# Kernel tuning notes

Measured on AMD Instinct MI355X. Metric: run time of the kernel, lower is better.

The kernel has to match this reference:

```python
import jax, jax.numpy as jnp
import numpy as np

B, A, N, G, F = 16, 256, 64, 64, 128  # batch, atoms, neighbors, gaussians, filters
CUTOFF = 5.0


def ssp(x):
    # shifted softplus: ln(0.5*e^x + 0.5)
    return jax.nn.softplus(x) - jnp.log(2.0).astype(x.dtype)


def setup_inputs() -> dict:
    key = jax.random.key(0)
    ks = jax.random.split(key, 10)
    x = jax.random.normal(ks[0], (B, A, F), jnp.float32)
    r_ij = jax.random.uniform(ks[1], (B, A, N), jnp.float32) * 6.0  # some beyond cutoff
    f_ij = jax.random.uniform(ks[2], (B, A, N, G), jnp.float32)  # gaussian-expanded dists
    neighbors = jax.random.randint(ks[3], (B, A, N), 0, A)
    pairwise_mask = (jax.random.uniform(ks[4], (B, A, N)) < 0.9).astype(jnp.float32)
    s = lambda fan: 1.0 / np.sqrt(fan)
    fw1 = jax.random.normal(ks[5], (G, F), jnp.float32) * s(G)
    fb1 = jnp.zeros((F,), jnp.float32)
    fw2 = jax.random.normal(ks[6], (F, F), jnp.float32) * s(F)
    fb2 = jnp.zeros((F,), jnp.float32)
    w_in2f = jax.random.normal(ks[7], (F, F), jnp.float32) * s(F)
    w_f2out = jax.random.normal(ks[8], (F, F), jnp.float32) * s(F)
    b_f2out = jnp.zeros((F,), jnp.float32)
    return {"x": x, "r_ij": r_ij, "f_ij": f_ij, "neighbors": neighbors,
            "pairwise_mask": pairwise_mask, "fw1": fw1, "fb1": fb1, "fw2": fw2,
            "fb2": fb2, "w_in2f": w_in2f, "w_f2out": w_f2out, "b_f2out": b_f2out}


def reference(x, r_ij, f_ij, neighbors, pairwise_mask,
              fw1, fb1, fw2, fb2, w_in2f, w_f2out, b_f2out):
    # filter network: Dense(G->F, ssp) -> Dense(F->F)
    W = ssp(jnp.einsum('bang,gf->banf', f_ij, fw1) + fb1)
    W = jnp.einsum('banf,fh->banh', W, fw2) + fb2  # [B,A,N,F]
    # cosine cutoff
    C = 0.5 * (jnp.cos(r_ij * (jnp.pi / CUTOFF)) + 1.0)
    C = C * (r_ij < CUTOFF).astype(r_ij.dtype)
    W = W * C[..., None]
    # in2f (no bias), then gather neighbor features along atom axis
    y = jnp.einsum('bad,df->baf', x, w_in2f)  # [B,A,F]
    bidx = jnp.arange(y.shape[0])[:, None, None]
    y_nbh = y[bidx, neighbors]  # [B,A,N,F]
    # filter-weight multiply + masked sum aggregate over neighbor axis
    y = jnp.sum(y_nbh * W * pairwise_mask[..., None], axis=2)  # [B,A,F]
    # f2out with shifted-softplus activation
    return ssp(jnp.einsum('baf,fo->bao', y, w_f2out) + b_f2out)
```

## Files before the change

### kernel.cpp

```cpp
#include <hip/hip_runtime.h>
#include <hip/hip_bf16.h>
#include <math.h>

#define B_ 16
#define A_ 256
#define N_ 64
#define G_ 64
#define F_ 128

typedef __attribute__((ext_vector_type(8))) short short8;
typedef __attribute__((ext_vector_type(4))) float floatx4;

__device__ __forceinline__ float ssp(float x) {
    const float t = __expf(-fabsf(x));
    return fmaxf(x, 0.0f) + __logf(1.0f + t) - 0.69314718055994531f;
}
__device__ __forceinline__ unsigned f2bf(float f) {
    union { float f; unsigned u; } v; v.f = f;
    v.u += 0x7fffu + ((v.u >> 16) & 1u);
    return v.u >> 16;
}
__device__ __forceinline__ float bf2f_lo(unsigned d) {
    union { unsigned i; float f; } v; v.i = d << 16; return v.f;
}
__device__ __forceinline__ float bf2f_hi(unsigned d) {
    union { unsigned i; float f; } v; v.i = d & 0xffff0000u; return v.f;
}

__global__ __launch_bounds__(256) void k0_repack(
    const float* __restrict__ fw1, const float* __restrict__ fw2,
    const float* __restrict__ win, const float* __restrict__ wout,
    unsigned short* __restrict__ fw1B, unsigned short* __restrict__ fw2B,
    unsigned short* __restrict__ winB, unsigned short* __restrict__ woutB)
{
    int idx = blockIdx.x * 1024 + threadIdx.x * 4;
    #pragma unroll
    for (int u = 0; u < 4; ++u, ++idx) {
        if (idx < 8192) {
            const int j  = idx & 7;
            const int l  = (idx >> 3) & 63;
            const int ks = (idx >> 9) & 1;
            const int tf = idx >> 10;
            const int g  = ks * 32 + (l >> 4) * 8 + j;
            const int f  = tf * 16 + (l & 15);
            fw1B[idx] = (unsigned short)f2bf(fw1[g * F_ + f]);
        } else {
            const int i2  = (idx - 8192) & 16383;
            const int sel = (idx - 8192) >> 14;
            const int j  = i2 & 7;
            const int l  = (i2 >> 3) & 63;
            const int ks = (i2 >> 9) & 3;
            const int tf = i2 >> 11;
            const int k  = ks * 32 + (l >> 4) * 8 + j;
            const int f  = tf * 16 + (l & 15);
            const float v = (sel == 0) ? fw2[k * F_ + f]
                          : (sel == 1) ? win[k * F_ + f]
                                       : wout[k * F_ + f];
            unsigned short* dst = (sel == 0) ? fw2B : (sel == 1) ? winB : woutB;
            dst[i2] = (unsigned short)f2bf(v);
        }
    }
}

__global__ __launch_bounds__(256) void in2f_gemm(
    const float* __restrict__ x, const unsigned short* __restrict__ winB,
    unsigned short* __restrict__ ypre)
{
    const int tid = threadIdx.x;
    const int w = tid >> 6, l = tid & 63, quad = l >> 4, c0 = l & 15;
    const int row = blockIdx.x * 64 + w * 16 + c0;

    short8 a[4];
    {
        const float* base = x + (size_t)row * F_ + quad * 8;
        #pragma unroll
        for (int ks = 0; ks < 4; ++ks) {
            const float4 v0 = *(const float4*)(base + ks * 32);
            const float4 v1 = *(const float4*)(base + ks * 32 + 4);
            short8 t;
            t[0] = (short)f2bf(v0.x); t[1] = (short)f2bf(v0.y);
            t[2] = (short)f2bf(v0.z); t[3] = (short)f2bf(v0.w);
            t[4] = (short)f2bf(v1.x); t[5] = (short)f2bf(v1.y);
            t[6] = (short)f2bf(v1.z); t[7] = (short)f2bf(v1.w);
            a[ks] = t;
        }
    }

    const short8* W8 = (const short8*)winB;
    floatx4 acc[8];
    #pragma unroll
    for (int tf = 0; tf < 8; ++tf) acc[tf] = (floatx4){0.f,0.f,0.f,0.f};
    #pragma unroll
    for (int ks = 0; ks < 4; ++ks)
        #pragma unroll
        for (int tf = 0; tf < 8; ++tf)
            acc[tf] = __builtin_amdgcn_mfma_f32_16x16x32_bf16(
                a[ks], W8[(tf * 4 + ks) * 64 + l], acc[tf], 0, 0, 0);

    #pragma unroll
    for (int r = 0; r < 4; ++r) {
        const int ro = blockIdx.x * 64 + w * 16 + quad * 4 + r;
        short8 s;
        #pragma unroll
        for (int tf = 0; tf < 8; ++tf) s[tf] = (short)f2bf(acc[tf][r]);
        *(short8*)&ypre[(size_t)ro * F_ + c0 * 8] = s;
    }
}

__global__ __launch_bounds__(512) void cfconv_kernel(
    const float* __restrict__ r_ij, const float* __restrict__ f_ij,
    const int*   __restrict__ nbrs, const float* __restrict__ mask,
    const float* __restrict__ fb1,  const float* __restrict__ fb2,
    const unsigned short* __restrict__ ypre,
    const unsigned short* __restrict__ fw1B,
    const unsigned short* __restrict__ fw2B,
    unsigned short* __restrict__ y_agg)
{
    __shared__ unsigned short s_w[24576];
    __shared__ short s_h1[N_ * F_];
    __shared__ float s_scale[N_];
    __shared__ int   s_nb[N_];
    __shared__ float s_red[4][F_];

    const int blk  = blockIdx.x;
    const int tid  = threadIdx.x;
    const int b    = blk >> 8;
    const int w    = tid >> 6;
    const int l    = tid & 63;
    const int quad = l >> 4;
    const int c0   = l & 15;
    const int rw   = w & 3;
    const int h    = w >> 2;

    {
        const uint4* w1 = (const uint4*)fw1B;
        const uint4* w2 = (const uint4*)fw2B;
        uint4* dst = (uint4*)s_w;
        #pragma unroll
        for (int i = 0; i < 6; ++i) {
            const int idx = tid + i * 512;
            dst[idx] = (idx < 1024) ? w1[idx] : w2[idx - 1024];
        }
    }
    if (h == 0 && l < 16) {
        const int n = rw * 16 + l;
        const float r = r_ij[(size_t)blk * N_ + n];
        const float c = (r < 5.0f)
            ? 0.5f * (__cosf(r * 0.62831853071795865f) + 1.0f)
            : 0.0f;
        s_scale[n] = c * mask[(size_t)blk * N_ + n];
        s_nb[n]    = nbrs[(size_t)blk * N_ + n];
    }

    short8 a1[2];
    {
        const float* base = f_ij + (size_t)blk * (N_ * G_)
                          + (size_t)(rw * 16 + c0) * G_ + quad * 8;
        #pragma unroll
        for (int ks = 0; ks < 2; ++ks) {
            const float4 v0 = *(const float4*)(base + ks * 32);
            const float4 v1 = *(const float4*)(base + ks * 32 + 4);
            short8 a;
            a[0] = (short)f2bf(v0.x); a[1] = (short)f2bf(v0.y);
            a[2] = (short)f2bf(v0.z); a[3] = (short)f2bf(v0.w);
            a[4] = (short)f2bf(v1.x); a[5] = (short)f2bf(v1.y);
            a[6] = (short)f2bf(v1.z); a[7] = (short)f2bf(v1.w);
            a1[ks] = a;
        }
    }
    __syncthreads();

    const short8* sw1 = (const short8*)s_w;
    const short8* sw2 = (const short8*)(s_w + 8192);

    floatx4 acc1[4];
    #pragma unroll
    for (int t = 0; t < 4; ++t) acc1[t] = (floatx4){0.f,0.f,0.f,0.f};
    #pragma unroll
    for (int ks = 0; ks < 2; ++ks)
        #pragma unroll
        for (int t = 0; t < 4; ++t) {
            const int tf = h * 4 + t;
            acc1[t] = __builtin_amdgcn_mfma_f32_16x16x32_bf16(
                a1[ks], sw1[(tf * 2 + ks) * 64 + l], acc1[t], 0, 0, 0);
        }

    #pragma unroll
    for (int t = 0; t < 4; ++t) {
        const int   tf    = h * 4 + t;
        const float bias  = fb1[tf * 16 + c0];
        const int   chunk = tf * 2 + (c0 >> 3);
        const int   o     = c0 & 7;
        #pragma unroll
        for (int r = 0; r < 4; ++r) {
            const int row_l = quad * 4 + r;
            const float v = ssp(acc1[t][r] + bias);
            s_h1[(rw * 16 + row_l) * F_ + ((chunk ^ row_l) * 8) + o] =
                (short)f2bf(v);
        }
    }
    __syncthreads();

    short8 a2[4];
    #pragma unroll
    for (int ks = 0; ks < 4; ++ks)
        a2[ks] = *(const short8*)&s_h1[(rw * 16 + c0) * F_
                                       + (((ks * 4 + quad) ^ c0) * 8)];

    float scl[4];
    uint2 yv[4];
    #pragma unroll
    for (int r = 0; r < 4; ++r) {
        const int n = rw * 16 + quad * 4 + r;
        scl[r] = s_scale[n];
        yv[r] = *(const uint2*)&ypre[(size_t)(b * A_ + s_nb[n]) * F_
                                     + c0 * 8 + h * 4];
    }

    floatx4 acc2[4];
    #pragma unroll
    for (int t = 0; t < 4; ++t) acc2[t] = (floatx4){0.f,0.f,0.f,0.f};
    #pragma unroll
    for (int ks = 0; ks < 4; ++ks)
        #pragma unroll
        for (int t = 0; t < 4; ++t) {
            const int tf = h * 4 + t;
            acc2[t] = __builtin_amdgcn_mfma_f32_16x16x32_bf16(
                a2[ks], sw2[(tf * 4 + ks) * 64 + l], acc2[t], 0, 0, 0);
        }

    float part[4];
    #pragma unroll
    for (int t = 0; t < 4; ++t) part[t] = 0.0f;
    #pragma unroll
    for (int r = 0; r < 4; ++r) {
        const unsigned d0 = yv[r].x, d1 = yv[r].y;
        part[0] = fmaf((acc2[0][r] + fb2[(h*4+0)*16+c0]) * scl[r], bf2f_lo(d0), part[0]);
        part[1] = fmaf((acc2[1][r] + fb2[(h*4+1)*16+c0]) * scl[r], bf2f_hi(d0), part[1]);
        part[2] = fmaf((acc2[2][r] + fb2[(h*4+2)*16+c0]) * scl[r], bf2f_lo(d1), part[2]);
        part[3] = fmaf((acc2[3][r] + fb2[(h*4+3)*16+c0]) * scl[r], bf2f_hi(d1), part[3]);
    }

    #pragma unroll
    for (int t = 0; t < 4; ++t) {
        part[t] += __shfl_xor(part[t], 16, 64);
        part[t] += __shfl_xor(part[t], 32, 64);
    }
    if (l < 16) {
        #pragma unroll
        for (int t = 0; t < 4; ++t)
            s_red[rw][(h * 4 + t) * 16 + l] = part[t];
    }
    __syncthreads();

    if (tid < F_) {
        const float v = s_red[0][tid] + s_red[1][tid]
                      + s_red[2][tid] + s_red[3][tid];
        y_agg[(size_t)blk * F_ + tid] = (unsigned short)f2bf(v);
    }
}

__global__ __launch_bounds__(256) void f2out_kernel(
    const unsigned short* __restrict__ y_agg,
    const unsigned short* __restrict__ woutB,
    const float* __restrict__ bias, float* __restrict__ out)
{
    const int tid = threadIdx.x;
    const int w = tid >> 6, l = tid & 63, quad = l >> 4, c0 = l & 15;
    const int row = blockIdx.x * 64 + w * 16 + c0;

    short8 a[4];
    #pragma unroll
    for (int ks = 0; ks < 4; ++ks)
        a[ks] = *(const short8*)&y_agg[(size_t)row * F_ + ks * 32 + quad * 8];

    const short8* W8 = (const short8*)woutB;
    floatx4 acc[8];
    #pragma unroll
    for (int tf = 0; tf < 8; ++tf) acc[tf] = (floatx4){0.f,0.f,0.f,0.f};
    #pragma unroll
    for (int ks = 0; ks < 4; ++ks)
        #pragma unroll
        for (int tf = 0; tf < 8; ++tf)
            acc[tf] = __builtin_amdgcn_mfma_f32_16x16x32_bf16(
                a[ks], W8[(tf * 4 + ks) * 64 + l], acc[tf], 0, 0, 0);

    #pragma unroll
    for (int tf = 0; tf < 8; ++tf) {
        const float bs = bias[tf * 16 + c0];
        #pragma unroll
        for (int r = 0; r < 4; ++r) {
            const int ro = blockIdx.x * 64 + w * 16 + quad * 4 + r;
            out[(size_t)ro * F_ + tf * 16 + c0] = ssp(acc[tf][r] + bs);
        }
    }
}

extern "C" void kernel_launch(void* const* d_in, const int* in_sizes, int n_in,
                              void* d_out, int out_size, void* d_ws, size_t ws_size,
                              hipStream_t stream) {
    const float* x        = (const float*)d_in[0];
    const float* r_ij     = (const float*)d_in[1];
    const float* f_ij     = (const float*)d_in[2];
    const int*   nbrs     = (const int*)  d_in[3];
    const float* mask     = (const float*)d_in[4];
    const float* fw1      = (const float*)d_in[5];
    const float* fb1      = (const float*)d_in[6];
    const float* fw2      = (const float*)d_in[7];
    const float* fb2      = (const float*)d_in[8];
    const float* w_in2f   = (const float*)d_in[9];
    const float* w_f2out  = (const float*)d_in[10];
    const float* b_f2out  = (const float*)d_in[11];
    float* out = (float*)d_out;

    unsigned short* ypre  = (unsigned short*)d_ws;
    unsigned short* fw1B  = ypre  + (size_t)B_ * A_ * F_;
    unsigned short* fw2B  = fw1B  + 8192;
    unsigned short* winB  = fw2B  + 16384;
    unsigned short* woutB = winB  + 16384;
    unsigned short* y_agg = woutB + 16384;

    k0_repack<<<56, 256, 0, stream>>>(
        fw1, fw2, w_in2f, w_f2out, fw1B, fw2B, winB, woutB);
    in2f_gemm<<<B_ * A_ / 64, 256, 0, stream>>>(x, winB, ypre);
    cfconv_kernel<<<B_ * A_, 512, 0, stream>>>(
        r_ij, f_ij, nbrs, mask, fb1, fb2, ypre, fw1B, fw2B, y_agg);
    f2out_kernel<<<B_ * A_ / 64, 256, 0, stream>>>(y_agg, woutB, b_f2out, out);
}
```

Baseline: 162.3 us.

## Process eight atoms per cfconv block to amortize weight staging and prefetch inputs

The cfconv kernel now loops over eight atoms per block instead of one. The 48KB of bf16 filter weights staged into LDS, and the bias values, are loaded once and reused across those atoms, which cuts repeated L2 weight traffic and per-block setup. The next atom's f_ij rows, cutoff scale and neighbor indices are prefetched into registers and a double-buffered LDS slot while the current atom's first GEMM runs. The grid shrinks eightfold, which lowers parallelism and makes each block work through its atoms serially with barriers between steps.

New measurement: 156.7 us (median of 2 runs). 3.4% less time.

```diff
diff --git a/kernel.cpp b/kernel.cpp
--- a/kernel.cpp
+++ b/kernel.cpp
@@ -7,6 +7,7 @@
 #define N_ 64
 #define G_ 64
 #define F_ 128
+#define APB 8
 
 typedef __attribute__((ext_vector_type(8))) short short8;
 typedef __attribute__((ext_vector_type(4))) float floatx4;
@@ -25,6 +26,14 @@
 }
 __device__ __forceinline__ float bf2f_hi(unsigned d) {
     union { unsigned i; float f; } v; v.i = d & 0xffff0000u; return v.f;
+}
+__device__ __forceinline__ short8 pack_bf8(const float4& v0, const float4& v1) {
+    short8 t;
+    t[0] = (short)f2bf(v0.x); t[1] = (short)f2bf(v0.y);
+    t[2] = (short)f2bf(v0.z); t[3] = (short)f2bf(v0.w);
+    t[4] = (short)f2bf(v1.x); t[5] = (short)f2bf(v1.y);
+    t[6] = (short)f2bf(v1.z); t[7] = (short)f2bf(v1.w);
+    return t;
 }
 
 __global__ __launch_bounds__(256) void k0_repack(
@@ -74,16 +83,9 @@
     {
         const float* base = x + (size_t)row * F_ + quad * 8;
         #pragma unroll
-        for (int ks = 0; ks < 4; ++ks) {
-            const float4 v0 = *(const float4*)(base + ks * 32);
-            const float4 v1 = *(const float4*)(base + ks * 32 + 4);
-            short8 t;
-            t[0] = (short)f2bf(v0.x); t[1] = (short)f2bf(v0.y);
-            t[2] = (short)f2bf(v0.z); t[3] = (short)f2bf(v0.w);
-            t[4] = (short)f2bf(v1.x); t[5] = (short)f2bf(v1.y);
-            t[6] = (short)f2bf(v1.z); t[7] = (short)f2bf(v1.w);
-            a[ks] = t;
-        }
+        for (int ks = 0; ks < 4; ++ks)
+            a[ks] = pack_bf8(*(const float4*)(base + ks * 32),
+                             *(const float4*)(base + ks * 32 + 4));
     }
 
     const short8* W8 = (const short8*)winB;
@@ -118,13 +120,11 @@
 {
     __shared__ unsigned short s_w[24576];
     __shared__ short s_h1[N_ * F_];
-    __shared__ float s_scale[N_];
-    __shared__ int   s_nb[N_];
+    __shared__ float s_scale[2][N_];
+    __shared__ int   s_nb[2][N_];
     __shared__ float s_red[4][F_];
 
-    const int blk  = blockIdx.x;
     const int tid  = threadIdx.x;
-    const int b    = blk >> 8;
     const int w    = tid >> 6;
     const int l    = tid & 63;
     const int quad = l >> 4;
@@ -132,6 +132,9 @@
     const int rw   = w & 3;
     const int h    = w >> 2;
 
+    const int abase = blockIdx.x * APB;
+    const int b     = abase >> 8;
+
     {
         const uint4* w1 = (const uint4*)fw1B;
         const uint4* w2 = (const uint4*)fw2B;
@@ -144,119 +147,143 @@
     }
     if (h == 0 && l < 16) {
         const int n = rw * 16 + l;
-        const float r = r_ij[(size_t)blk * N_ + n];
+        const float r = r_ij[(size_t)abase * N_ + n];
         const float c = (r < 5.0f)
             ? 0.5f * (__cosf(r * 0.62831853071795865f) + 1.0f)
             : 0.0f;
-        s_scale[n] = c * mask[(size_t)blk * N_ + n];
-        s_nb[n]    = nbrs[(size_t)blk * N_ + n];
-    }
-
-    short8 a1[2];
+        s_scale[0][n] = c * mask[(size_t)abase * N_ + n];
+        s_nb[0][n]    = nbrs[(size_t)abase * N_ + n];
+    }
+    float4 pf[4];
     {
-        const float* base = f_ij + (size_t)blk * (N_ * G_)
+        const float* base = f_ij + (size_t)abase * (N_ * G_)
                           + (size_t)(rw * 16 + c0) * G_ + quad * 8;
-        #pragma unroll
-        for (int ks = 0; ks < 2; ++ks) {
-            const float4 v0 = *(const float4*)(base + ks * 32);
-            const float4 v1 = *(const float4*)(base + ks * 32 + 4);
-            short8 a;
-            a[0] = (short)f2bf(v0.x); a[1] = (short)f2bf(v0.y);
-            a[2] = (short)f2bf(v0.z); a[3] = (short)f2bf(v0.w);
-            a[4] = (short)f2bf(v1.x); a[5] = (short)f2bf(v1.y);
-            a[6] = (short)f2bf(v1.z); a[7] = (short)f2bf(v1.w);
-            a1[ks] = a;
-        }
+        pf[0] = *(const float4*)(base);
+        pf[1] = *(const float4*)(base + 4);
+        pf[2] = *(const float4*)(base + 32);
+        pf[3] = *(const float4*)(base + 36);
+    }
+    float fb1v[4], fb2v[4];
+    #pragma unroll
+    for (int t = 0; t < 4; ++t) {
+        fb1v[t] = fb1[(h * 4 + t) * 16 + c0];
+        fb2v[t] = fb2[(h * 4 + t) * 16 + c0];
     }
     __syncthreads();
 
     const short8* sw1 = (const short8*)s_w;
     const short8* sw2 = (const short8*)(s_w + 8192);
-
-    floatx4 acc1[4];
-    #pragma unroll
-    for (int t = 0; t < 4; ++t) acc1[t] = (floatx4){0.f,0.f,0.f,0.f};
-    #pragma unroll
-    for (int ks = 0; ks < 2; ++ks)
+    const unsigned short* yb = ypre + (size_t)b * A_ * F_;
+
+    for (int i = 0; i < APB; ++i) {
+        const int atom = abase + i;
+        const int buf  = i & 1;
+
+        short8 a1[2];
+        a1[0] = pack_bf8(pf[0], pf[1]);
+        a1[1] = pack_bf8(pf[2], pf[3]);
+
+        floatx4 acc1[4];
+        #pragma unroll
+        for (int t = 0; t < 4; ++t) acc1[t] = (floatx4){0.f,0.f,0.f,0.f};
+        #pragma unroll
+        for (int ks = 0; ks < 2; ++ks)
+            #pragma unroll
+            for (int t = 0; t < 4; ++t) {
+                const int tf = h * 4 + t;
+                acc1[t] = __builtin_amdgcn_mfma_f32_16x16x32_bf16(
+                    a1[ks], sw1[(tf * 2 + ks) * 64 + l], acc1[t], 0, 0, 0);
+            }
+
+        if (i + 1 < APB) {
+            const float* base = f_ij + (size_t)(atom + 1) * (N_ * G_)
+                              + (size_t)(rw * 16 + c0) * G_ + quad * 8;
+            pf[0] = *(const float4*)(base);
+            pf[1] = *(const float4*)(base + 4);
+            pf[2] = *(const float4*)(base + 32);
+            pf[3] = *(const float4*)(base + 36);
+            if (h == 0 && l < 16) {
+                const int n = rw * 16 + l;
+                const float r = r_ij[(size_t)(atom + 1) * N_ + n];
+                const float c = (r < 5.0f)
+                    ? 0.5f * (__cosf(r * 0.62831853071795865f) + 1.0f)
+                    : 0.0f;
+                s_scale[buf ^ 1][n] = c * mask[(size_t)(atom + 1) * N_ + n];
+                s_nb[buf ^ 1][n]    = nbrs[(size_t)(atom + 1) * N_ + n];
+            }
+        }
+
         #pragma unroll
         for (int t = 0; t < 4; ++t) {
-            const int tf = h * 4 + t;
-            acc1[t] = __builtin_amdgcn_mfma_f32_16x16x32_bf16(
-                a1[ks], sw1[(tf * 2 + ks) * 64 + l], acc1[t], 0, 0, 0);
-        }
-
-    #pragma unroll
-    for (int t = 0; t < 4; ++t) {
-        const int   tf    = h * 4 + t;
-        const float bias  = fb1[tf * 16 + c0];
-        const int   chunk = tf * 2 + (c0 >> 3);
-        const int   o     = c0 & 7;
+            const int   tf    = h * 4 + t;
+            const int   chunk = tf * 2 + (c0 >> 3);
+            const int   o     = c0 & 7;
+            #pragma unroll
+            for (int r = 0; r < 4; ++r) {
+                const int row_l = quad * 4 + r;
+                const float v = ssp(acc1[t][r] + fb1v[t]);
+                s_h1[(rw * 16 + row_l) * F_ + ((chunk ^ row_l) * 8) + o] =
+                    (short)f2bf(v);
+            }
+        }
+        __syncthreads();
+
+        short8 a2[4];
+        #pragma unroll
+        for (int ks = 0; ks < 4; ++ks)
+            a2[ks] = *(const short8*)&s_h1[(rw * 16 + c0) * F_
+                                           + (((ks * 4 + quad) ^ c0) * 8)];
+
+        float scl[4];
+        uint2 yv[4];
         #pragma unroll
         for (int r = 0; r < 4; ++r) {
-            const int row_l = quad * 4 + r;
-            const float v = ssp(acc1[t][r] + bias);
-            s_h1[(rw * 16 + row_l) * F_ + ((chunk ^ row_l) * 8) + o] =
-                (short)f2bf(v);
-        }
-    }
-    __syncthreads();
-
-    short8 a2[4];
-    #pragma unroll
-    for (int ks = 0; ks < 4; ++ks)
-        a2[ks] = *(const short8*)&s_h1[(rw * 16 + c0) * F_
-                                       + (((ks * 4 + quad) ^ c0) * 8)];
-
-    float scl[4];
-    uint2 yv[4];
-    #pragma unroll
-    for (int r = 0; r < 4; ++r) {
-        const int n = rw * 16 + quad * 4 + r;
-        scl[r] = s_scale[n];
-        yv[r] = *(const uint2*)&ypre[(size_t)(b * A_ + s_nb[n]) * F_
-                                     + c0 * 8 + h * 4];
-    }
-
-    floatx4 acc2[4];
-    #pragma unroll
-    for (int t = 0; t < 4; ++t) acc2[t] = (floatx4){0.f,0.f,0.f,0.f};
-    #pragma unroll
-    for (int ks = 0; ks < 4; ++ks)
+            const int n = rw * 16 + quad * 4 + r;
+            scl[r] = s_scale[buf][n];
+            yv[r] = *(const uint2*)&yb[(size_t)s_nb[buf][n] * F_
+                                       + c0 * 8 + h * 4];
+        }
+
+        floatx4 acc2[4];
+        #pragma unroll
+        for (int t = 0; t < 4; ++t) acc2[t] = (floatx4){0.f,0.f,0.f,0.f};
+        #pragma unroll
+        for (int ks = 0; ks < 4; ++ks)
+            #pragma unroll
+            for (int t = 0; t < 4; ++t) {
+                const int tf = h * 4 + t;
+                acc2[t] = __builtin_amdgcn_mfma_f32_16x16x32_bf16(
+                    a2[ks], sw2[(tf * 4 + ks) * 64 + l], acc2[t], 0, 0, 0);
+            }
+
+        float part[4];
+        #pragma unroll
+        for (int t = 0; t < 4; ++t) part[t] = 0.0f;
+        #pragma unroll
+        for (int r = 0; r < 4; ++r) {
+            const unsigned d0 = yv[r].x, d1 = yv[r].y;
+            part[0] = fmaf((acc2[0][r] + fb2v[0]) * scl[r], bf2f_lo(d0), part[0]);
+            part[1] = fmaf((acc2[1][r] + fb2v[1]) * scl[r], bf2f_hi(d0), part[1]);
+            part[2] = fmaf((acc2[2][r] + fb2v[2]) * scl[r], bf2f_lo(d1), part[2]);
+            part[3] = fmaf((acc2[3][r] + fb2v[3]) * scl[r], bf2f_hi(d1), part[3]);
+        }
         #pragma unroll
         for (int t = 0; t < 4; ++t) {
-            const int tf = h * 4 + t;
-            acc2[t] = __builtin_amdgcn_mfma_f32_16x16x32_bf16(
-                a2[ks], sw2[(tf * 4 + ks) * 64 + l], acc2[t], 0, 0, 0);
-        }
-
-    float part[4];
-    #pragma unroll
-    for (int t = 0; t < 4; ++t) part[t] = 0.0f;
-    #pragma unroll
-    for (int r = 0; r < 4; ++r) {
-        const unsigned d0 = yv[r].x, d1 = yv[r].y;
-        part[0] = fmaf((acc2[0][r] + fb2[(h*4+0)*16+c0]) * scl[r], bf2f_lo(d0), part[0]);
-        part[1] = fmaf((acc2[1][r] + fb2[(h*4+1)*16+c0]) * scl[r], bf2f_hi(d0), part[1]);
-        part[2] = fmaf((acc2[2][r] + fb2[(h*4+2)*16+c0]) * scl[r], bf2f_lo(d1), part[2]);
-        part[3] = fmaf((acc2[3][r] + fb2[(h*4+3)*16+c0]) * scl[r], bf2f_hi(d1), part[3]);
-    }
-
-    #pragma unroll
-    for (int t = 0; t < 4; ++t) {
-        part[t] += __shfl_xor(part[t], 16, 64);
-        part[t] += __shfl_xor(part[t], 32, 64);
-    }
-    if (l < 16) {
-        #pragma unroll
-        for (int t = 0; t < 4; ++t)
-            s_red[rw][(h * 4 + t) * 16 + l] = part[t];
-    }
-    __syncthreads();
-
-    if (tid < F_) {
-        const float v = s_red[0][tid] + s_red[1][tid]
-                      + s_red[2][tid] + s_red[3][tid];
-        y_agg[(size_t)blk * F_ + tid] = (unsigned short)f2bf(v);
+            part[t] += __shfl_xor(part[t], 16, 64);
+            part[t] += __shfl_xor(part[t], 32, 64);
+        }
+        if (l < 16) {
+            #pragma unroll
+            for (int t = 0; t < 4; ++t)
+                s_red[rw][(h * 4 + t) * 16 + l] = part[t];
+        }
+        __syncthreads();
+
+        if (tid < F_) {
+            const float v = s_red[0][tid] + s_red[1][tid]
+                          + s_red[2][tid] + s_red[3][tid];
+            y_agg[(size_t)atom * F_ + tid] = (unsigned short)f2bf(v);
+        }
     }
 }
 
@@ -323,7 +350,7 @@
     k0_repack<<<56, 256, 0, stream>>>(
         fw1, fw2, w_in2f, w_f2out, fw1B, fw2B, winB, woutB);
     in2f_gemm<<<B_ * A_ / 64, 256, 0, stream>>>(x, winB, ypre);
-    cfconv_kernel<<<B_ * A_, 512, 0, stream>>>(
+    cfconv_kernel<<<B_ * A_ / APB, 512, 0, stream>>>(
         r_ij, f_ij, nbrs, mask, fb1, fb2, ypre, fw1B, fw2B, y_agg);
     f2out_kernel<<<B_ * A_ / 64, 256, 0, stream>>>(y_agg, woutB, b_f2out, out);
 }
```
